# Kernel optimization log

Measured on AMD Instinct MI355X. Metric: run time of the kernel, lower is better.

Reference implementation:

```python
import jax, jax.numpy as jnp
import numpy as np


def _conv(x, w, stride):
    # Conv2d(k=3, stride, padding=1, bias=False), NCHW/OIHW
    return jax.lax.conv_general_dilated(
        x, w, (stride, stride), ((1, 1), (1, 1)),
        dimension_numbers=('NCHW', 'OIHW', 'NCHW'))


def _bn_silu(x, g, b, m, v):
    # BatchNorm2d (inference) + SiLU, fused elementwise
    scale = (g * jax.lax.rsqrt(v + 1e-5))[None, :, None, None]
    y = (x - m[None, :, None, None]) * scale + b[None, :, None, None]
    return y * jax.nn.sigmoid(y)


def _ss2d(x, in_w, dt_w, dt_b, B_w, C_w, A_log, D, out_w):
    # Low-rank 2D selective scan over flattened spatial tokens.
    Bn, C, H, W = x.shape
    L = H * W
    xt = x.reshape(Bn, C, L).transpose(0, 2, 1)            # [B,L,C]
    u = jnp.einsum('blc,rc->blr', xt, in_w)                # low-rank input [B,L,R]
    dt = jax.nn.softplus(jnp.einsum('blc,rc->blr', xt, dt_w) + dt_b)
    Bt = jnp.einsum('blc,nc->bln', xt, B_w)                # [B,L,N]
    Ct = jnp.einsum('blc,nc->bln', xt, C_w)                # [B,L,N]
    A = -jnp.exp(A_log)                                    # [R,N], stable (negative)

    def step(h, inp):
        u_t, dt_t, b_t, c_t = inp                          # [B,R],[B,R],[B,N],[B,N]
        dA = jnp.exp(dt_t[..., None] * A)                  # [B,R,N]
        h = dA * h + (dt_t[..., None] * b_t[:, None, :]) * u_t[..., None]
        y = jnp.einsum('brn,bn->br', h, c_t)               # [B,R]
        return h, (h, y)

    R, N = A_log.shape
    h0 = jnp.zeros((Bn, R, N), x.dtype)
    xs = (u.transpose(1, 0, 2), dt.transpose(1, 0, 2),
          Bt.transpose(1, 0, 2), Ct.transpose(1, 0, 2))
    _, (hs, ys) = jax.lax.scan(step, h0, xs)               # hs:[L,B,R,N] ys:[L,B,R]
    y = ys.transpose(1, 0, 2) + D * u                      # skip term D*u
    out = jnp.einsum('blr,cr->blc', y, out_w)              # project back to C
    x_out = (xt + out).transpose(0, 2, 1).reshape(Bn, C, H, W)
    state_seq = hs.transpose(1, 0, 2, 3)                   # [B,L,R,N]
    return x_out, state_seq


def setup_inputs() -> dict:
    key = jax.random.key(0)
    ks = jax.random.split(key, 24)
    f = jax.random.normal
    B, Cin, H, W = 8, 32, 112, 112
    E, R, N, NB = 64, 32, 64, 3
    inp = {}
    inp['x'] = f(ks[0], (B, Cin, H, W), jnp.float32)
    # stem
    inp['stem_w'] = f(ks[1], (E, Cin, 3, 3)) * 0.05
    inp['stem_g'] = 1.0 + 0.1 * f(ks[2], (E,))
    inp['stem_b'] = 0.1 * f(ks[3], (E,))
    inp['stem_m'] = 0.1 * f(ks[4], (E,))
    inp['stem_v'] = 1.0 + 0.1 * jax.random.uniform(ks[5], (E,))
    # SS2D blocks (stacked over num_blocks)
    inp['blk_in_w'] = f(ks[6], (NB, R, E)) * 0.1
    inp['blk_dt_w'] = f(ks[7], (NB, R, E)) * 0.05
    inp['blk_dt_b'] = f(ks[8], (NB, R)) * 0.1 - 2.0
    inp['blk_B_w'] = f(ks[9], (NB, N, E)) * 0.1
    inp['blk_C_w'] = f(ks[10], (NB, N, E)) * 0.1
    inp['blk_A_log'] = jnp.log(1.0 + jax.random.uniform(ks[11], (NB, R, N)) * 4.0)
    inp['blk_D'] = f(ks[12], (NB, R)) * 0.1
    inp['blk_out_w'] = f(ks[13], (NB, E, R)) * 0.1
    # down p4
    C4, C5 = 2 * E, 4 * E
    inp['p4_w'] = f(ks[14], (C4, E, 3, 3)) * 0.05
    inp['p4_g'] = 1.0 + 0.1 * f(ks[15], (C4,))
    inp['p4_b'] = 0.1 * f(ks[16], (C4,))
    inp['p4_m'] = 0.1 * f(ks[17], (C4,))
    inp['p4_v'] = 1.0 + 0.1 * jax.random.uniform(ks[18], (C4,))
    # down p5
    inp['p5_w'] = f(ks[19], (C5, C4, 3, 3)) * 0.05
    inp['p5_g'] = 1.0 + 0.1 * f(ks[20], (C5,))
    inp['p5_b'] = 0.1 * f(ks[21], (C5,))
    inp['p5_m'] = 0.1 * f(ks[22], (C5,))
    inp['p5_v'] = 1.0 + 0.1 * jax.random.uniform(ks[23], (C5,))
    return inp


def reference(x, stem_w, stem_g, stem_b, stem_m, stem_v,
              blk_in_w, blk_dt_w, blk_dt_b, blk_B_w, blk_C_w,
              blk_A_log, blk_D, blk_out_w,
              p4_w, p4_g, p4_b, p4_m, p4_v,
              p5_w, p5_g, p5_b, p5_m, p5_v):
    x = _bn_silu(_conv(x, stem_w, 2), stem_g, stem_b, stem_m, stem_v)
    states = []
    for i in range(blk_in_w.shape[0]):
        x, s = _ss2d(x, blk_in_w[i], blk_dt_w[i], blk_dt_b[i],
                     blk_B_w[i], blk_C_w[i], blk_A_log[i], blk_D[i], blk_out_w[i])
        states.append(s)
    p3 = x
    p4 = _bn_silu(_conv(p3, p4_w, 2), p4_g, p4_b, p4_m, p4_v)
    p5 = _bn_silu(_conv(p4, p5_w, 2), p5_g, p5_b, p5_m, p5_v)
    return (p3, p4, p5, jnp.stack(states))
```

## Files before the change

kernel.cpp:

```cpp
#include <hip/hip_runtime.h>
#include <cstdint>
#include <cstddef>

#define RFL(x) __builtin_amdgcn_readfirstlane(x)

constexpr int E  = 64;
constexpr int Rr = 32;
constexpr int Nn = 64;
constexpr int Lt = 3136;
constexpr int NC = 28;
constexpr int CL = 112;
constexpr int PD = 192;

__global__ __launch_bounds__(256) void k_setup(
    const float* __restrict__ in_w, const float* __restrict__ dt_w,
    const float* __restrict__ B_w, const float* __restrict__ C_w,
    const float* __restrict__ stem_w, const float* __restrict__ p4_w,
    const float* __restrict__ p5_w,
    float* __restrict__ wT, float* __restrict__ w3s,
    float* __restrict__ w34, float* __restrict__ w35) {
  int idx = blockIdx.x * 256 + threadIdx.x;
  if (idx < 36864) {
    int o = idx % PD; int c = (idx / PD) & 63; int i = idx / (PD * 64);
    float v;
    if (o < 32)       v = in_w[(i * 32 + o) * 64 + c];
    else if (o < 64)  v = dt_w[(i * 32 + (o - 32)) * 64 + c];
    else if (o < 128) v = B_w[(i * 64 + (o - 64)) * 64 + c];
    else              v = C_w[(i * 64 + (o - 128)) * 64 + c];
    wT[idx] = v;
  } else if (idx < 36864 + 18432) {
    int j = idx - 36864;
    int co = j % 64; int k = (j / 64) % 9; int ci = j / (64 * 9);
    w3s[j] = stem_w[((size_t)co * 32 + ci) * 9 + k];
  } else if (idx < 36864 + 18432 + 73728) {
    int j = idx - 36864 - 18432;
    int co = j % 128; int k = (j / 128) % 9; int ci = j / (128 * 9);
    w34[j] = p4_w[((size_t)co * 64 + ci) * 9 + k];
  } else if (idx < 36864 + 18432 + 73728 + 294912) {
    int j = idx - 36864 - 18432 - 73728;
    int co = j % 256; int k = (j / 256) % 9; int ci = j / (256 * 9);
    w35[j] = p5_w[((size_t)co * 128 + ci) * 9 + k];
  }
}

template<int CIN, int COUT, int HIN, int WIN>
__global__ __launch_bounds__(256) void k_conv6(const float* __restrict__ x,
    const float* __restrict__ w3, const float* __restrict__ g, const float* __restrict__ bb,
    const float* __restrict__ m, const float* __restrict__ vv, float* __restrict__ out) {
  constexpr int HOUT = HIN / 2, WOUT = WIN / 2;
  constexpr int OWT = 7;
  constexpr int GWX = WOUT / OWT;
  constexpr int CIW = CIN / 4;
  __shared__ float tbuf[4][64][8];

  int t = blockIdx.x;
  int b = t & 7; t >>= 3;
  int oh = t % HOUT; t /= HOUT;
  int gx = t % GWX; int cog = t / GWX;
  int lane = threadIdx.x & 63;
  int ws = RFL(threadIdx.x >> 6);
  int co = cog * 64 + lane;
  int iwb = gx * 14;
  int ih0 = oh * 2 - 1;
  bool leftok = (iwb > 0);

  const float* xb = x + (size_t)b * CIN * HIN * WIN;
  float acc[OWT];
#pragma unroll
  for (int o = 0; o < OWT; ++o) acc[o] = 0.f;

  int ci0 = ws * CIW;
#pragma unroll 2
  for (int cc = 0; cc < CIW; ++cc) {
    int ci = ci0 + cc;
    const float* xp = xb + (size_t)ci * HIN * WIN;
    const float* wr = w3 + ((size_t)(ci * 9)) * COUT + co;
    float wk[9];
#pragma unroll
    for (int k = 0; k < 9; ++k) wk[k] = wr[(size_t)k * COUT];
#pragma unroll
    for (int kh = 0; kh < 3; ++kh) {
      int ih = ih0 + kh;
      if (ih >= 0) {
        const float* xr = xp + (size_t)ih * WIN + iwb;
        float tp[15];
        tp[0] = leftok ? xr[-1] : 0.f;
#pragma unroll
        for (int j = 1; j < 15; ++j) tp[j] = xr[j - 1];
#pragma unroll
        for (int o = 0; o < OWT; ++o) {
          acc[o] = fmaf(tp[2 * o],     wk[kh * 3 + 0], acc[o]);
          acc[o] = fmaf(tp[2 * o + 1], wk[kh * 3 + 1], acc[o]);
          acc[o] = fmaf(tp[2 * o + 2], wk[kh * 3 + 2], acc[o]);
        }
      }
    }
  }
#pragma unroll
  for (int o = 0; o < OWT; ++o) tbuf[ws][lane][o] = acc[o];
  __syncthreads();

  for (int i = threadIdx.x; i < 64 * OWT; i += 256) {
    int cl = i / OWT, o = i - cl * OWT;
    float s = tbuf[0][cl][o] + tbuf[1][cl][o] + tbuf[2][cl][o] + tbuf[3][cl][o];
    int c2 = cog * 64 + cl;
    float scale = g[c2] * rsqrtf(vv[c2] + 1e-5f);
    float yv = (s - m[c2]) * scale + bb[c2];
    out[(((size_t)(b * COUT + c2)) * HOUT + oh) * WOUT + gx * OWT + o] =
        yv / (1.f + __expf(-yv));
  }
}

__global__ __launch_bounds__(256) void k_proj(const float* __restrict__ xin,
    const float* __restrict__ wT, const float* __restrict__ dt_b, float* __restrict__ P) {
  __shared__ float sm[64 * 196];
  int b = blockIdx.x & 7, tl = blockIdx.x >> 3;
  int l0 = tl * 64;
  int tid = threadIdx.x;
  for (int k = 0; k < 16; ++k) {
    int idx = k * 256 + tid; int c = idx >> 6, li = idx & 63;
    sm[c * 65 + li] = xin[(size_t)(b * 64 + c) * Lt + l0 + li];
  }
  __syncthreads();
  int tok = tid & 63;
  int og = RFL(tid >> 6);
  const float* wbase = wT + og * 48;
  float acc[48];
#pragma unroll
  for (int j = 0; j < 48; ++j) acc[j] = 0.f;
  for (int c = 0; c < 64; ++c) {
    float xv = sm[c * 65 + tok];
    const float4* w4 = (const float4*)(wbase + c * PD);
#pragma unroll
    for (int j = 0; j < 12; ++j) {
      float4 wv = __ldg(w4 + j);
      acc[4 * j + 0] = fmaf(xv, wv.x, acc[4 * j + 0]);
      acc[4 * j + 1] = fmaf(xv, wv.y, acc[4 * j + 1]);
      acc[4 * j + 2] = fmaf(xv, wv.z, acc[4 * j + 2]);
      acc[4 * j + 3] = fmaf(xv, wv.w, acc[4 * j + 3]);
    }
  }
  __syncthreads();
#pragma unroll
  for (int j = 0; j < 48; ++j) {
    int o = og * 48 + j;
    float v = acc[j];
    if (o >= 32 && o < 64) {
      v += dt_b[o - 32];
      v = fmaxf(v, 0.f) + log1pf(__expf(-fabsf(v)));
    }
    sm[tok * 196 + o] = v;
  }
  __syncthreads();
  float* dst = P + ((size_t)(b * Lt + l0)) * PD;
#pragma unroll
  for (int it = 0; it < 12; ++it) {
    int f = it * 1024 + tid * 4;
    int tk = f / 192;
    float4 v = *(const float4*)(&sm[tk * 196 + (f - tk * 192)]);
    *(float4*)(dst + f) = v;
  }
}

__global__ __launch_bounds__(256) void k_scan1(const float* __restrict__ P,
    const float* __restrict__ A_log, float* __restrict__ hfin, float* __restrict__ Pc) {
  __shared__ float xl[16][132];
  int bid = blockIdx.x;
  int b = bid & 7; int rest = bid >> 3;
  int c = rest % NC; int rg = rest / NC;
  int ws = RFL(threadIdx.x >> 6);
  int r = rg * 4 + ws;
  int n = threadIdx.x & 63;
  float a = -__expf(A_log[r * 64 + n]);
  const float* base = P + ((size_t)(b * Lt + c * CL)) * PD;
  int tl = threadIdx.x >> 4;
  int colb = (threadIdx.x & 15) * 8;
  float h = 0.f, sdt = 0.f;
  for (int s0 = 0; s0 < CL; s0 += 16) {
    __syncthreads();
    const float4* src = (const float4*)(base + (size_t)(s0 + tl) * PD + colb);
    float4 v0 = src[0], v1 = src[1];
    *(float4*)(&xl[tl][colb]) = v0;
    *(float4*)(&xl[tl][colb + 4]) = v1;
    __syncthreads();
#pragma unroll
    for (int tt = 0; tt < 16; ++tt) {
      float dt = xl[tt][32 + r];
      float u  = xl[tt][r];
      float bt = xl[tt][64 + n];
      h = fmaf(__expf(dt * a), h, (dt * u) * bt);
      sdt += dt;
    }
  }
  int o = ((b * 32 + r) * NC + c) * 64 + n;
  hfin[o] = h;
  Pc[o] = __expf(a * sdt);
}

__global__ __launch_bounds__(256) void k_scan3(const float* __restrict__ P,
    const float* __restrict__ A_log, const float* __restrict__ hfin,
    const float* __restrict__ Pcp, const float* __restrict__ Dp,
    float* __restrict__ states, float* __restrict__ y) {
  __shared__ float xl[16][196];
  __shared__ __align__(16) float ylds[4][16][68];
  int bid = blockIdx.x;
  int b = bid & 7; int rest = bid >> 3;
  int c = rest % NC; int rg = rest / NC;
  int ws = RFL(threadIdx.x >> 6);
  int r = rg * 4 + ws;
  int n = threadIdx.x & 63;
  float a = -__expf(A_log[r * 64 + n]);
  float Dr = Dp[r];
  const float* base = P + ((size_t)(b * Lt + c * CL)) * PD;
  float h = 0.f;
  {
    int bp = ((b * 32 + r) * NC) * 64 + n;
    for (int cc = 0; cc < c; ++cc)
      h = fmaf(Pcp[bp + cc * 64], h, hfin[bp + cc * 64]);
  }
  float* st = states + ((size_t)(b * Lt + c * CL) * 32 + r) * 64 + n;
  float* yrow = y + (size_t)(b * 32 + r) * Lt + c * CL;
  int tl = threadIdx.x >> 4;
  int colb = (threadIdx.x & 15) * 12;
  for (int s0 = 0; s0 < CL; s0 += 16) {
    __syncthreads();
    const float4* src = (const float4*)(base + (size_t)(s0 + tl) * PD + colb);
    float4 v0 = src[0], v1 = src[1], v2 = src[2];
    *(float4*)(&xl[tl][colb])     = v0;
    *(float4*)(&xl[tl][colb + 4]) = v1;
    *(float4*)(&xl[tl][colb + 8]) = v2;
    __syncthreads();
#pragma unroll
    for (int tt = 0; tt < 16; ++tt) {
      float dt = xl[tt][32 + r];
      float u  = xl[tt][r];
      float bt = xl[tt][64 + n];
      float ct = xl[tt][128 + n];
      h = fmaf(__expf(dt * a), h, (dt * u) * bt);
      __builtin_nontemporal_store(h, st + (size_t)(s0 + tt) * 2048);
      ylds[ws][tt][n] = h * ct;
    }
    if (n < 16) {
      const float4* rp = (const float4*)(&ylds[ws][n][0]);
      float a0 = 0.f, a1 = 0.f, a2 = 0.f, a3 = 0.f;
#pragma unroll
      for (int k = 0; k < 16; ++k) {
        float4 pv = rp[k];
        a0 += pv.x; a1 += pv.y; a2 += pv.z; a3 += pv.w;
      }
      float sum = (a0 + a1) + (a2 + a3);
      float uu = xl[n][r];
      yrow[s0 + n] = sum + Dr * uu;
    }
  }
}

__global__ __launch_bounds__(256) void k_outproj(const float* __restrict__ xin,
    const float* __restrict__ y, const float* __restrict__ ow, float* __restrict__ xout) {
  __shared__ float ylds[32 * 64];
  int b = blockIdx.x & 7, tl = blockIdx.x >> 3;
  int l0 = tl * 64;
  int tid = threadIdx.x;
  for (int k = 0; k < 8; ++k) {
    int idx = k * 256 + tid; int r = idx >> 6, li = idx & 63;
    ylds[r * 64 + li] = y[(size_t)(b * 32 + r) * Lt + l0 + li];
  }
  __syncthreads();
  int li = tid & 63, cg = RFL(tid >> 6);
  for (int cc = 0; cc < 16; ++cc) {
    int ci = cg * 16 + cc;
    float acc = xin[(size_t)(b * 64 + ci) * Lt + l0 + li];
    const float4* w4 = (const float4*)(ow + ci * 32);
#pragma unroll
    for (int r4 = 0; r4 < 8; ++r4) {
      float4 wv = __ldg(w4 + r4);
      acc = fmaf(ylds[(r4 * 4 + 0) * 64 + li], wv.x, acc);
      acc = fmaf(ylds[(r4 * 4 + 1) * 64 + li], wv.y, acc);
      acc = fmaf(ylds[(r4 * 4 + 2) * 64 + li], wv.z, acc);
      acc = fmaf(ylds[(r4 * 4 + 3) * 64 + li], wv.w, acc);
    }
    xout[(size_t)(b * 64 + ci) * Lt + l0 + li] = acc;
  }
}

extern "C" void kernel_launch(void* const* d_in, const int* in_sizes, int n_in,
                              void* d_out, int out_size, void* d_ws, size_t ws_size,
                              hipStream_t stream) {
  const float* x      = (const float*)d_in[0];
  const float* stem_w = (const float*)d_in[1];
  const float* stem_g = (const float*)d_in[2];
  const float* stem_b = (const float*)d_in[3];
  const float* stem_m = (const float*)d_in[4];
  const float* stem_v = (const float*)d_in[5];
  const float* in_w   = (const float*)d_in[6];
  const float* dt_w   = (const float*)d_in[7];
  const float* dt_b   = (const float*)d_in[8];
  const float* B_w    = (const float*)d_in[9];
  const float* C_w    = (const float*)d_in[10];
  const float* A_log  = (const float*)d_in[11];
  const float* Dp     = (const float*)d_in[12];
  const float* out_w  = (const float*)d_in[13];
  const float* p4_w   = (const float*)d_in[14];
  const float* p4_g   = (const float*)d_in[15];
  const float* p4_b   = (const float*)d_in[16];
  const float* p4_m   = (const float*)d_in[17];
  const float* p4_v   = (const float*)d_in[18];
  const float* p5_w   = (const float*)d_in[19];
  const float* p5_g   = (const float*)d_in[20];
  const float* p5_b   = (const float*)d_in[21];
  const float* p5_m   = (const float*)d_in[22];
  const float* p5_v   = (const float*)d_in[23];

  float* out = (float*)d_out;
  float* wsf = (float*)d_ws;

  float* p3out = out;
  float* p4out = out + 1605632;
  float* p5out = out + 2408448;
  float* stout = out + 2809856;

  float* x0    = wsf;
  float* x1    = wsf + 1605632;
  float* Pb    = wsf + 3211264;
  float* yb    = wsf + 8028160;
  float* hfin  = wsf + 8830976;
  float* Pc    = wsf + 9289728;
  float* wT    = wsf + 9748480;
  float* w3s   = wsf + 9785344;
  float* w34   = wsf + 9803776;
  float* w35   = wsf + 9877504;

  k_setup<<<1656, 256, 0, stream>>>(in_w, dt_w, B_w, C_w, stem_w, p4_w, p5_w,
                                    wT, w3s, w34, w35);

  k_conv6<32, 64, 112, 112><<<3584, 256, 0, stream>>>(
      x, w3s, stem_g, stem_b, stem_m, stem_v, x0);

  const float* xi = x0;
  for (int i = 0; i < 3; ++i) {
    k_proj<<<392, 256, 0, stream>>>(xi, wT + i * 64 * PD, dt_b + i * 32, Pb);
    k_scan1<<<1792, 256, 0, stream>>>(Pb, A_log + i * 2048, hfin, Pc);
    k_scan3<<<1792, 256, 0, stream>>>(Pb, A_log + i * 2048, hfin, Pc, Dp + i * 32,
                                      stout + (size_t)i * 51380224, yb);
    float* dst = (i == 2) ? p3out : ((i == 0) ? x1 : x0);
    k_outproj<<<392, 256, 0, stream>>>(xi, yb, out_w + i * 2048, dst);
    xi = dst;
  }

  k_conv6<64, 128, 56, 56><<<1792, 256, 0, stream>>>(
      p3out, w34, p4_g, p4_b, p4_m, p4_v, p4out);
  k_conv6<128, 256, 28, 28><<<896, 256, 0, stream>>>(
      p4out, w35, p5_g, p5_b, p5_m, p5_v, p5out);
}
```

Baseline: 404.9 us.

## Rework chunked selective scan with finer chunks and vectorized per-thread state updates

Doubles the number of scan chunks by halving chunk length. The second scan pass now has each thread own four N-states for one R row, 16 R rows per block. This lets the dominant state-sequence writes go out as 16-byte nontemporal stores. The y reduction uses wave shuffles instead of an LDS partial-sum pass, and y is staged in LDS for coalesced row writes. The x1 intermediate moves into the not-yet-written last-block state region of the output, shrinking the workspace. The cost is more serial chunk-prefix iterations per block and more first-pass blocks.

```diff
diff --git a/kernel.cpp b/kernel.cpp
--- a/kernel.cpp
+++ b/kernel.cpp
@@ -3,13 +3,16 @@
 #include <cstddef>
 
 #define RFL(x) __builtin_amdgcn_readfirstlane(x)
+
+typedef float floatx4 __attribute__((ext_vector_type(4)));
 
 constexpr int E  = 64;
 constexpr int Rr = 32;
 constexpr int Nn = 64;
 constexpr int Lt = 3136;
-constexpr int NC = 28;
-constexpr int CL = 112;
+constexpr int NC = 56;
+constexpr int CL = 56;
+constexpr int TT = 14;
 constexpr int PD = 192;
 
 __global__ __launch_bounds__(256) void k_setup(
@@ -63,8 +66,8 @@
   int iwb = gx * 14;
   int ih0 = oh * 2 - 1;
   bool leftok = (iwb > 0);
-
   const float* xb = x + (size_t)b * CIN * HIN * WIN;
+
   float acc[OWT];
 #pragma unroll
   for (int o = 0; o < OWT; ++o) acc[o] = 0.f;
@@ -164,7 +167,7 @@
 
 __global__ __launch_bounds__(256) void k_scan1(const float* __restrict__ P,
     const float* __restrict__ A_log, float* __restrict__ hfin, float* __restrict__ Pc) {
-  __shared__ float xl[16][132];
+  __shared__ float xl[TT][132];
   int bid = blockIdx.x;
   int b = bid & 7; int rest = bid >> 3;
   int c = rest % NC; int rg = rest / NC;
@@ -173,18 +176,16 @@
   int n = threadIdx.x & 63;
   float a = -__expf(A_log[r * 64 + n]);
   const float* base = P + ((size_t)(b * Lt + c * CL)) * PD;
-  int tl = threadIdx.x >> 4;
-  int colb = (threadIdx.x & 15) * 8;
   float h = 0.f, sdt = 0.f;
-  for (int s0 = 0; s0 < CL; s0 += 16) {
+  for (int s0 = 0; s0 < CL; s0 += TT) {
     __syncthreads();
-    const float4* src = (const float4*)(base + (size_t)(s0 + tl) * PD + colb);
-    float4 v0 = src[0], v1 = src[1];
-    *(float4*)(&xl[tl][colb]) = v0;
-    *(float4*)(&xl[tl][colb + 4]) = v1;
+    for (int j = threadIdx.x; j < TT * 32; j += 256) {
+      int tl = j >> 5, c4 = (j & 31) * 4;
+      *(float4*)(&xl[tl][c4]) = *(const float4*)(base + (size_t)(s0 + tl) * PD + c4);
+    }
     __syncthreads();
 #pragma unroll
-    for (int tt = 0; tt < 16; ++tt) {
+    for (int tt = 0; tt < TT; ++tt) {
       float dt = xl[tt][32 + r];
       float u  = xl[tt][r];
       float bt = xl[tt][64 + n];
@@ -201,57 +202,70 @@
     const float* __restrict__ A_log, const float* __restrict__ hfin,
     const float* __restrict__ Pcp, const float* __restrict__ Dp,
     float* __restrict__ states, float* __restrict__ y) {
-  __shared__ float xl[16][196];
-  __shared__ __align__(16) float ylds[4][16][68];
+  __shared__ __align__(16) float xl[TT][200];
+  __shared__ float yl[16][60];
   int bid = blockIdx.x;
   int b = bid & 7; int rest = bid >> 3;
-  int c = rest % NC; int rg = rest / NC;
+  int c = rest % NC; int rg2 = rest / NC;
   int ws = RFL(threadIdx.x >> 6);
-  int r = rg * 4 + ws;
-  int n = threadIdx.x & 63;
-  float a = -__expf(A_log[r * 64 + n]);
+  int lane = threadIdx.x & 63;
+  int rsub = lane >> 4, nq = lane & 15;
+  int rl = ws * 4 + rsub;
+  int r = rg2 * 16 + rl;
+  int n0 = nq * 4;
+  float a[4], h[4];
+#pragma unroll
+  for (int j = 0; j < 4; ++j) {
+    a[j] = -__expf(A_log[r * 64 + n0 + j]);
+    h[j] = 0.f;
+  }
+  {
+    size_t bp = ((size_t)(b * 32 + r) * NC) * 64 + n0;
+    for (int cc = 0; cc < c; ++cc) {
+      float4 pc = *(const float4*)(Pcp + bp + (size_t)cc * 64);
+      float4 hf = *(const float4*)(hfin + bp + (size_t)cc * 64);
+      h[0] = fmaf(pc.x, h[0], hf.x);
+      h[1] = fmaf(pc.y, h[1], hf.y);
+      h[2] = fmaf(pc.z, h[2], hf.z);
+      h[3] = fmaf(pc.w, h[3], hf.w);
+    }
+  }
   float Dr = Dp[r];
   const float* base = P + ((size_t)(b * Lt + c * CL)) * PD;
-  float h = 0.f;
-  {
-    int bp = ((b * 32 + r) * NC) * 64 + n;
-    for (int cc = 0; cc < c; ++cc)
-      h = fmaf(Pcp[bp + cc * 64], h, hfin[bp + cc * 64]);
-  }
-  float* st = states + ((size_t)(b * Lt + c * CL) * 32 + r) * 64 + n;
-  float* yrow = y + (size_t)(b * 32 + r) * Lt + c * CL;
-  int tl = threadIdx.x >> 4;
-  int colb = (threadIdx.x & 15) * 12;
-  for (int s0 = 0; s0 < CL; s0 += 16) {
+  float* st = states + ((size_t)(b * Lt + c * CL)) * 2048 + r * 64 + n0;
+  for (int s0 = 0; s0 < CL; s0 += TT) {
     __syncthreads();
-    const float4* src = (const float4*)(base + (size_t)(s0 + tl) * PD + colb);
-    float4 v0 = src[0], v1 = src[1], v2 = src[2];
-    *(float4*)(&xl[tl][colb])     = v0;
-    *(float4*)(&xl[tl][colb + 4]) = v1;
-    *(float4*)(&xl[tl][colb + 8]) = v2;
+    for (int j = threadIdx.x; j < TT * 48; j += 256) {
+      int tl = j / 48, c4 = (j - tl * 48) * 4;
+      *(float4*)(&xl[tl][c4]) = *(const float4*)(base + (size_t)(s0 + tl) * PD + c4);
+    }
     __syncthreads();
 #pragma unroll
-    for (int tt = 0; tt < 16; ++tt) {
+    for (int tt = 0; tt < TT; ++tt) {
       float dt = xl[tt][32 + r];
       float u  = xl[tt][r];
-      float bt = xl[tt][64 + n];
-      float ct = xl[tt][128 + n];
-      h = fmaf(__expf(dt * a), h, (dt * u) * bt);
-      __builtin_nontemporal_store(h, st + (size_t)(s0 + tt) * 2048);
-      ylds[ws][tt][n] = h * ct;
-    }
-    if (n < 16) {
-      const float4* rp = (const float4*)(&ylds[ws][n][0]);
-      float a0 = 0.f, a1 = 0.f, a2 = 0.f, a3 = 0.f;
-#pragma unroll
-      for (int k = 0; k < 16; ++k) {
-        float4 pv = rp[k];
-        a0 += pv.x; a1 += pv.y; a2 += pv.z; a3 += pv.w;
-      }
-      float sum = (a0 + a1) + (a2 + a3);
-      float uu = xl[n][r];
-      yrow[s0 + n] = sum + Dr * uu;
-    }
+      float4 bt = *(const float4*)(&xl[tt][64 + n0]);
+      float4 ct = *(const float4*)(&xl[tt][128 + n0]);
+      float du = dt * u;
+      h[0] = fmaf(__expf(dt * a[0]), h[0], du * bt.x);
+      h[1] = fmaf(__expf(dt * a[1]), h[1], du * bt.y);
+      h[2] = fmaf(__expf(dt * a[2]), h[2], du * bt.z);
+      h[3] = fmaf(__expf(dt * a[3]), h[3], du * bt.w);
+      floatx4 hv = {h[0], h[1], h[2], h[3]};
+      __builtin_nontemporal_store(hv, (floatx4*)(st + (size_t)(s0 + tt) * 2048));
+      float p = h[0] * ct.x + h[1] * ct.y + h[2] * ct.z + h[3] * ct.w;
+      p += __shfl_xor(p, 1);
+      p += __shfl_xor(p, 2);
+      p += __shfl_xor(p, 4);
+      p += __shfl_xor(p, 8);
+      if (nq == 0) yl[rl][s0 + tt] = p + Dr * u;
+    }
+  }
+  __syncthreads();
+  float* yb2 = y + ((size_t)(b * 32 + rg2 * 16)) * Lt + c * CL;
+  for (int i = threadIdx.x; i < 16 * CL; i += 256) {
+    int rr = i / CL, t = i - rr * CL;
+    yb2[(size_t)rr * Lt + t] = yl[rr][t];
   }
 }
 
@@ -319,16 +333,17 @@
   float* p5out = out + 2408448;
   float* stout = out + 2809856;
 
+  float* x1 = stout + (size_t)2 * 51380224;
+
   float* x0    = wsf;
-  float* x1    = wsf + 1605632;
-  float* Pb    = wsf + 3211264;
-  float* yb    = wsf + 8028160;
-  float* hfin  = wsf + 8830976;
-  float* Pc    = wsf + 9289728;
-  float* wT    = wsf + 9748480;
-  float* w3s   = wsf + 9785344;
-  float* w34   = wsf + 9803776;
-  float* w35   = wsf + 9877504;
+  float* Pb    = wsf + 1605632;
+  float* yb    = wsf + 6422528;
+  float* hfin  = wsf + 7225344;
+  float* Pc    = wsf + 8142848;
+  float* wT    = wsf + 9060352;
+  float* w3s   = wsf + 9097216;
+  float* w34   = wsf + 9115648;
+  float* w35   = wsf + 9189376;
 
   k_setup<<<1656, 256, 0, stream>>>(in_w, dt_w, B_w, C_w, stem_w, p4_w, p5_w,
                                     wT, w3s, w34, w35);
@@ -339,9 +354,9 @@
   const float* xi = x0;
   for (int i = 0; i < 3; ++i) {
     k_proj<<<392, 256, 0, stream>>>(xi, wT + i * 64 * PD, dt_b + i * 32, Pb);
-    k_scan1<<<1792, 256, 0, stream>>>(Pb, A_log + i * 2048, hfin, Pc);
-    k_scan3<<<1792, 256, 0, stream>>>(Pb, A_log + i * 2048, hfin, Pc, Dp + i * 32,
-                                      stout + (size_t)i * 51380224, yb);
+    k_scan1<<<3584, 256, 0, stream>>>(Pb, A_log + i * 2048, hfin, Pc);
+    k_scan3<<<896, 256, 0, stream>>>(Pb, A_log + i * 2048, hfin, Pc, Dp + i * 32,
+                                     stout + (size_t)i * 51380224, yb);
     float* dst = (i == 2) ? p3out : ((i == 0) ? x1 : x0);
     k_outproj<<<392, 256, 0, stream>>>(xi, yb, out_w + i * 2048, dst);
     xi = dst;
```

New measurement: 413.4 us. 1.02x slower.
